# Kernel tuning notes

Hardware: AMD Instinct MI355X
Metric: run time of the kernel (lower is better)

Reference implementation:

```python
import jax, jax.numpy as jnp
import numpy as np

STRIDES = (8, 16, 32)
C = 80          # num_classes
KA = 3          # anchors per level
TOPK = 100      # per-level top-k
CONF_TH = 0.001
NMS_TH = 0.5
INPUT_SIZE = 2048
ANCHOR_SIZES = np.array([[[10, 13], [16, 30], [33, 23]],
                         [[30, 61], [62, 45], [59, 119]],
                         [[116, 90], [156, 198], [373, 326]]], dtype=np.float32)


def make_anchors(level):
    # Mirrors YOLOv3.create_grid: torch.meshgrid default is 'ij' indexing.
    fmp = INPUT_SIZE // STRIDES[level]
    gy, gx = np.meshgrid(np.arange(fmp), np.arange(fmp), indexing='ij')
    grid_xy = np.stack([gx, gy], axis=-1).reshape(-1, 1, 2).astype(np.float32)  # [HW,1,2]
    grid_xy = np.broadcast_to(grid_xy, (fmp * fmp, KA, 2))
    wh = np.broadcast_to(ANCHOR_SIZES[level][None], (fmp * fmp, KA, 2))
    return jnp.asarray(np.concatenate([grid_xy, wh], axis=-1).reshape(-1, 4))  # [HW*KA,4]


def setup_inputs() -> dict:
    key = jax.random.key(0)
    ks = jax.random.split(key, 9)
    d = {}
    for lvl in range(3):
        N = (INPUT_SIZE // STRIDES[lvl]) ** 2 * KA
        d[f"conf_pred_{lvl + 1}"] = jax.random.normal(ks[3 * lvl], (N, 1), jnp.float32)
        d[f"cls_pred_{lvl + 1}"] = jax.random.normal(ks[3 * lvl + 1], (N, C), jnp.float32)
        d[f"reg_pred_{lvl + 1}"] = jax.random.normal(ks[3 * lvl + 2], (N, 4), jnp.float32) * 0.5
        d[f"anchors_{lvl + 1}"] = make_anchors(lvl)
    return d


def _level(conf, cls, reg, anchors, stride):
    # scores = sigmoid(objectness) * softmax(class logits), flattened over (anchor, class)
    prob = jax.nn.sigmoid(conf) * jax.nn.softmax(cls, axis=-1)      # [N,C]
    scores, idx = jax.lax.top_k(prob.reshape(-1), TOPK)             # [TOPK]
    valid = scores > CONF_TH
    a_idx = idx // C
    labels = idx % C
    r = reg[a_idx]                                                  # [TOPK,4]
    a = anchors[a_idx]                                              # [TOPK,4]
    # decode_boxes: xy = (sigmoid(txy)+grid)*stride ; wh = exp(twh)*anchor_wh
    xy = (jax.nn.sigmoid(r[:, :2]) + a[:, :2]) * stride
    wh = jnp.exp(r[:, 2:]) * a[:, 2:]
    boxes = jnp.concatenate([xy - 0.5 * wh, xy + 0.5 * wh], axis=-1)  # x1y1x2y2
    return scores, labels, boxes, valid


def reference(conf_pred_1, cls_pred_1, reg_pred_1,
              conf_pred_2, cls_pred_2, reg_pred_2,
              conf_pred_3, cls_pred_3, reg_pred_3,
              anchors_1, anchors_2, anchors_3):
    levels = [(conf_pred_1, cls_pred_1, reg_pred_1, anchors_1, STRIDES[0]),
              (conf_pred_2, cls_pred_2, reg_pred_2, anchors_2, STRIDES[1]),
              (conf_pred_3, cls_pred_3, reg_pred_3, anchors_3, STRIDES[2])]
    parts = [_level(*lv) for lv in levels]
    scores = jnp.concatenate([p[0] for p in parts])   # [3*TOPK]
    labels = jnp.concatenate([p[1] for p in parts])
    boxes = jnp.concatenate([p[2] for p in parts], axis=0)
    valid = jnp.concatenate([p[3] for p in parts])

    # Sort all candidates by score descending (greedy NMS order)
    order = jnp.argsort(-scores)
    scores, labels, boxes, valid = scores[order], labels[order], boxes[order], valid[order]

    x1, y1, x2, y2 = boxes[:, 0], boxes[:, 1], boxes[:, 2], boxes[:, 3]
    areas = (x2 - x1) * (y2 - y1)
    xx1 = jnp.maximum(x1[:, None], x1[None, :])
    yy1 = jnp.maximum(y1[:, None], y1[None, :])
    xx2 = jnp.minimum(x2[:, None], x2[None, :])
    yy2 = jnp.minimum(y2[:, None], y2[None, :])
    w = jnp.maximum(1e-10, xx2 - xx1)
    h = jnp.maximum(1e-10, yy2 - yy1)
    inter = w * h
    iou = inter / (areas[:, None] + areas[None, :] - inter)

    K = scores.shape[0]
    idxr = jnp.arange(K)
    # class-wise suppression: only same-label, lower-scored boxes can be suppressed
    sup_cond = (iou > NMS_TH) & (labels[:, None] == labels[None, :]) & (idxr[None, :] > idxr[:, None])

    def body(i, keep):
        return keep & ~(sup_cond[i] & keep[i])

    keep = jax.lax.fori_loop(0, K, body, valid)

    boxes_n = jnp.clip(boxes / INPUT_SIZE, 0.0, 1.0)
    out = jnp.concatenate([boxes_n, scores[:, None], labels.astype(jnp.float32)[:, None]], axis=1)
    return jnp.where(keep[:, None], out, 0.0)   # [3*TOPK, 6] = (x1,y1,x2,y2,score,label)
```

## Files before the change

### kernel.cpp

```cpp
#include <hip/hip_runtime.h>
#include <math.h>
#include <stdint.h>

#define NBUCKET 4096
#define NCOPY   8
#define CAP     16384
#define QCAP    4096
#define STAGE   4096
#define FCAP    1024
#define TOPK    100
#define NLVL    3
#define NCLS    80

#define PA_G1 1024
#define PA_G2 256
#define PA_G3 64
#define CK_G1 192
#define CK_G2 48
#define CK_G3 12

__global__ void passA_kernel(const float* __restrict__ conf1, const float* __restrict__ cls1,
                             const float* __restrict__ conf2, const float* __restrict__ cls2,
                             const float* __restrict__ conf3, const float* __restrict__ cls3,
                             int n1, int n2, int n3,
                             unsigned int* __restrict__ ghist,
                             float* __restrict__ amax)
{
    const float* conf; const float* cls; int nA, nb, b;
    unsigned int* gh; float* am;
    if (blockIdx.x < PA_G1) {
        b = blockIdx.x; conf = conf1; cls = cls1; nA = n1; nb = PA_G1;
        gh = ghist; am = amax;
    } else if (blockIdx.x < PA_G1 + PA_G2) {
        b = blockIdx.x - PA_G1; conf = conf2; cls = cls2; nA = n2; nb = PA_G2;
        gh = ghist + NCOPY * NBUCKET; am = amax + n1;
    } else {
        b = blockIdx.x - PA_G1 - PA_G2; conf = conf3; cls = cls3; nA = n3; nb = PA_G3;
        gh = ghist + 2 * NCOPY * NBUCKET; am = amax + n1 + n2;
    }

    __shared__ unsigned int sh[NBUCKET];
    for (int i = threadIdx.x; i < NBUCKET; i += 256) sh[i] = 0;
    __syncthreads();

    int sub = threadIdx.x & 15;
    int g16 = threadIdx.x >> 4;
    int nChunk = nA >> 4;
    for (int ch = b; ch < nChunk; ch += nb) {
        int a = (ch << 4) + g16;
        float cv  = conf[a];
        float sig = 1.0f / (1.0f + expf(-cv));
        const float* row = cls + (size_t)a * NCLS + sub;
        float c0 = row[0], c1 = row[16], c2 = row[32], c3 = row[48], c4 = row[64];
        float m = fmaxf(fmaxf(fmaxf(c0, c1), fmaxf(c2, c3)), c4);
#pragma unroll
        for (int o = 8; o >= 1; o >>= 1) m = fmaxf(m, __shfl_xor(m, o, 16));
        float s = ((expf(c0 - m) + expf(c1 - m)) + (expf(c2 - m) + expf(c3 - m))) + expf(c4 - m);
#pragma unroll
        for (int o = 8; o >= 1; o >>= 1) s += __shfl_xor(s, o, 16);
        float inv = sig / s;
        if (sub == 0) {
            am[a] = inv;
            unsigned bk = __float_as_uint(inv) >> 18;
            if (bk > NBUCKET - 1) bk = NBUCKET - 1;
            atomicAdd(&sh[bk], 1u);
        }
    }
    __syncthreads();
    unsigned int* g = gh + (b & (NCOPY - 1)) * NBUCKET;
    for (int i = threadIdx.x; i < NBUCKET; i += 256) {
        unsigned v = sh[i];
        if (v) atomicAdd(&g[i], v);
    }
}

__global__ void scan_kernel(const unsigned int* __restrict__ ghist,
                            unsigned int* __restrict__ thresh,
                            unsigned int* __restrict__ ccount)
{
    int lvl = blockIdx.x;
    const unsigned int* h0 = ghist + lvl * NCOPY * NBUCKET;
    __shared__ unsigned int h[NBUCKET];
    __shared__ unsigned int ps[256];
    int t = threadIdx.x;
    if (t == 0) ccount[lvl] = 0;
    for (int bb = t; bb < NBUCKET; bb += 256) {
        unsigned s = 0;
        for (int c = 0; c < NCOPY; c++) s += h0[c * NBUCKET + bb];
        h[bb] = s;
    }
    __syncthreads();
    unsigned cs = 0;
#pragma unroll
    for (int i = 0; i < 16; i++) cs += h[NBUCKET - 1 - (t * 16 + i)];
    ps[t] = cs;
    __syncthreads();
    for (int o = 1; o < 256; o <<= 1) {
        unsigned v = (t >= o) ? ps[t - o] : 0u;
        __syncthreads();
        ps[t] += v;
        __syncthreads();
    }
    unsigned incl = ps[t], excl = incl - cs;
    if (excl < TOPK && incl >= TOPK) {
        unsigned cum = excl, B = 0;
        for (int i = 0; i < 16; i++) {
            int bb = NBUCKET - 1 - (t * 16 + i);
            cum += h[bb];
            if (cum >= TOPK) { B = (unsigned)bb; break; }
        }
        thresh[lvl] = B << 18;
    }
}

__global__ void compact_kernel(const float* __restrict__ conf1, const float* __restrict__ cls1,
                               const float* __restrict__ conf2, const float* __restrict__ cls2,
                               const float* __restrict__ conf3, const float* __restrict__ cls3,
                               int n1, int n2, int n3,
                               const unsigned int* __restrict__ thresh,
                               const float* __restrict__ amax,
                               unsigned int* __restrict__ ccount,
                               float* __restrict__ cscore,
                               unsigned int* __restrict__ cidx)
{
    const float* conf; const float* cls; int bl, lvl; const float* am;
    if (blockIdx.x < CK_G1)              { lvl = 0; bl = blockIdx.x;               conf = conf1; cls = cls1; am = amax; }
    else if (blockIdx.x < CK_G1 + CK_G2) { lvl = 1; bl = blockIdx.x - CK_G1;       conf = conf2; cls = cls2; am = amax + n1; }
    else                                 { lvl = 2; bl = blockIdx.x - CK_G1 - CK_G2; conf = conf3; cls = cls3; am = amax + n1 + n2; }

    __shared__ int qn;
    __shared__ int queue[QCAP];
    if (threadIdx.x == 0) qn = 0;
    __syncthreads();

    unsigned T = thresh[lvl];
    int idx4 = bl * 256 + threadIdx.x;
    const float4* am4 = (const float4*)am;
    float4 v = am4[idx4];
    float vv[4] = {v.x, v.y, v.z, v.w};
#pragma unroll
    for (int j = 0; j < 4; j++) {
        if (__float_as_uint(vv[j]) >= T) {
            int p = atomicAdd(&qn, 1);
            if (p < QCAP) queue[p] = idx4 * 4 + j;
        }
    }
    __syncthreads();
    int qcnt = min(qn, QCAP);
    int grp = threadIdx.x >> 4;
    int sub = threadIdx.x & 15;
    float*        csl = cscore + lvl * CAP;
    unsigned int* cil = cidx   + lvl * CAP;
    for (int q = grp; q < qcnt; q += 16) {
        int a = queue[q];
        float cv  = conf[a];
        float sig = 1.0f / (1.0f + expf(-cv));
        const float* row = cls + (size_t)a * NCLS + sub;
        float c0 = row[0], c1 = row[16], c2 = row[32], c3 = row[48], c4 = row[64];
        float m = fmaxf(fmaxf(fmaxf(c0, c1), fmaxf(c2, c3)), c4);
#pragma unroll
        for (int o = 8; o >= 1; o >>= 1) m = fmaxf(m, __shfl_xor(m, o, 16));
        float e0 = expf(c0 - m), e1 = expf(c1 - m), e2 = expf(c2 - m),
              e3 = expf(c3 - m), e4 = expf(c4 - m);
        float s = ((e0 + e1) + (e2 + e3)) + e4;
#pragma unroll
        for (int o = 8; o >= 1; o >>= 1) s += __shfl_xor(s, o, 16);
        float inv = sig / s;
        float e[5] = {e0, e1, e2, e3, e4};
#pragma unroll
        for (int k = 0; k < 5; k++) {
            float p = e[k] * inv;
            if (e[k] == 1.0f || __float_as_uint(p) >= T) {
                unsigned pos = atomicAdd(&ccount[lvl], 1u);
                if (pos < CAP) {
                    csl[pos] = p;
                    cil[pos] = (unsigned)(a * NCLS + sub + 16 * k);
                }
            }
        }
    }
}

__global__ __launch_bounds__(1024, 4) void select_kernel(
    const float* __restrict__ cscore, const unsigned int* __restrict__ cidx,
    const unsigned int* __restrict__ ccount,
    const unsigned int* __restrict__ thresh,
    float* __restrict__ sel_sc, int* __restrict__ sel_ix)
{
    int lvl = blockIdx.x;
    int tid = threadIdx.x;
    __shared__ float        q_sc[STAGE];
    __shared__ unsigned int q_ix[STAGE];
    __shared__ unsigned int subh[4096];
    __shared__ unsigned int ps[1024];
    __shared__ unsigned int kthr_s;
    __shared__ int          fcnt;
    __shared__ float        f_sc[FCAP];
    __shared__ unsigned int f_ix[FCAP];

    int cnt = min((int)ccount[lvl], CAP);
    const float*        sc = cscore + lvl * CAP;
    const unsigned int* ix = cidx   + lvl * CAP;
    int n = min(cnt, STAGE);
    unsigned B12 = (thresh[lvl] >> 18) << 12;

    for (int i = tid; i < 4096; i += 1024) subh[i] = 0;
    if (tid == 0) fcnt = 0;
    for (int c = tid; c < n; c += 1024) { q_sc[c] = sc[c]; q_ix[c] = ix[c]; }
    if (tid < TOPK) { sel_sc[lvl * TOPK + tid] = -1e30f; sel_ix[lvl * TOPK + tid] = 0; }
    __syncthreads();

    for (int c = tid; c < cnt; c += 1024) {
        float v = (c < n) ? q_sc[c] : sc[c];
        unsigned rel = (__float_as_uint(v) >> 6) - B12;
        if (rel > 4095u) rel = 4095u;
        atomicAdd(&subh[rel], 1u);
    }
    __syncthreads();

    unsigned cs = 0;
#pragma unroll
    for (int i = 0; i < 4; i++) cs += subh[4095 - 4 * tid - i];
    ps[tid] = cs;
    __syncthreads();
    for (int o = 1; o < 1024; o <<= 1) {
        unsigned v = (tid >= o) ? ps[tid - o] : 0u;
        __syncthreads();
        ps[tid] += v;
        __syncthreads();
    }
    {
        unsigned incl = ps[tid], excl = incl - cs;
        if (excl < TOPK && incl >= TOPK) {
            unsigned cum = excl;
            for (int i = 0; i < 4; i++) {
                int sb = 4095 - 4 * tid - i;
                cum += subh[sb];
                if (cum >= TOPK) { kthr_s = (B12 + (unsigned)sb) << 6; break; }
            }
        }
    }
    __syncthreads();
    unsigned kthr = kthr_s;

    for (int c = tid; c < cnt; c += 1024) {
        float v; unsigned vi;
        if (c < n) { v = q_sc[c]; vi = q_ix[c]; }
        else       { v = sc[c];   vi = ix[c];   }
        if (__float_as_uint(v) >= kthr) {
            int p = atomicAdd(&fcnt, 1);
            if (p < FCAP) { f_sc[p] = v; f_ix[p] = vi; }
        }
    }
    __syncthreads();
    int fn = min(fcnt, FCAP);

    for (int c = tid; c < fn; c += 1024) {
        float    my  = f_sc[c];
        unsigned myi = f_ix[c];
        int rank = 0;
        for (int k = 0; k < fn; k++) {
            float v = f_sc[k];
            rank += (v > my) || (v == my && f_ix[k] < myi);
        }
        if (rank < TOPK) {
            sel_sc[lvl * TOPK + rank] = my;
            sel_ix[lvl * TOPK + rank] = (int)myi;
        }
    }
}

__device__ __forceinline__ float rlf(float x, int l)
{
    return __uint_as_float((unsigned)__builtin_amdgcn_readlane((int)__float_as_uint(x), l));
}
__device__ __forceinline__ int rli(int x, int l)
{
    return __builtin_amdgcn_readlane(x, l);
}
__device__ __forceinline__ unsigned long long rl64(unsigned long long x, int b)
{
    unsigned lo = (unsigned)__builtin_amdgcn_readlane((int)(unsigned)x, b);
    unsigned hi = (unsigned)__builtin_amdgcn_readlane((int)(unsigned)(x >> 32), b);
    return ((unsigned long long)hi << 32) | lo;
}

__global__ void prep_kernel(
    const float* __restrict__ reg1, const float* __restrict__ anch1,
    const float* __restrict__ reg2, const float* __restrict__ anch2,
    const float* __restrict__ reg3, const float* __restrict__ anch3,
    const float* __restrict__ sel_sc, const int* __restrict__ sel_ix,
    float* __restrict__ t_score, float* __restrict__ t_box,
    int* __restrict__ t_label, int* __restrict__ t_valid)
{
    int tid  = threadIdx.x;
    int lane = tid & 63;

    float sg[5];
#pragma unroll
    for (int g = 0; g < 5; g++) {
        int k = g * 64 + lane;
        sg[g] = (k < 300) ? sel_sc[k] : -INFINITY;
    }

    float my = (tid < 300) ? sel_sc[tid] : -INFINITY;
    int rank = 0;
#pragma unroll
    for (int g = 0; g < 5; g++) {
        int base = g * 64;
#pragma unroll 1
        for (int ii = 0; ii < 64; ii++) {
            float v = rlf(sg[g], ii);
            int k = base + ii;
            rank += (v > my) || (v == my && k < tid);
        }
    }

    if (tid < 300) {
        int lvl = tid / TOPK;
        const float* reg = lvl == 0 ? reg1 : (lvl == 1 ? reg2 : reg3);
        const float* anc = lvl == 0 ? anch1 : (lvl == 1 ? anch2 : anch3);
        float stride = lvl == 0 ? 8.0f : (lvl == 1 ? 16.0f : 32.0f);
        int  idx = sel_ix[tid];
        int a   = idx / NCLS;
        int lab = idx % NCLS;
        float r0 = reg[4 * a + 0], r1 = reg[4 * a + 1], r2 = reg[4 * a + 2], r3 = reg[4 * a + 3];
        float a0 = anc[4 * a + 0], a1 = anc[4 * a + 1], a2 = anc[4 * a + 2], a3 = anc[4 * a + 3];
        float cx = (1.0f / (1.0f + expf(-r0)) + a0) * stride;
        float cy = (1.0f / (1.0f + expf(-r1)) + a1) * stride;
        float w  = expf(r2) * a2;
        float h  = expf(r3) * a3;
        t_score[rank]       = my;
        t_box[4 * rank + 0] = cx - 0.5f * w;
        t_box[4 * rank + 1] = cy - 0.5f * h;
        t_box[4 * rank + 2] = cx + 0.5f * w;
        t_box[4 * rank + 3] = cy + 0.5f * h;
        t_label[rank] = lab;
        t_valid[rank] = my > 0.001f;
    }
}

__global__ void sup_kernel(const float* __restrict__ t_box,
                           const int* __restrict__ t_label,
                           unsigned long long* __restrict__ sup_ws)
{
    int tid  = threadIdx.x;
    int lane = tid & 63;
    int w    = tid >> 6;
    int rbase = 20 * blockIdx.x;

    float bx1 = 0, by1 = 0, bx2 = 0, by2 = 0, areaj = 0;
    int labj = -1;
    if (tid < 300) {
        bx1 = t_box[4 * tid + 0]; by1 = t_box[4 * tid + 1];
        bx2 = t_box[4 * tid + 2]; by2 = t_box[4 * tid + 3];
        labj = t_label[tid];
        areaj = (bx2 - bx1) * (by2 - by1);
    }

    float rx1 = 0, ry1 = 0, rx2 = 0, ry2 = 0, rar = 1.0f;
    int rlab = -9;
    int r = rbase + lane;
    if (lane < 20 && r < 300) {
        rx1 = t_box[4 * r + 0]; ry1 = t_box[4 * r + 1];
        rx2 = t_box[4 * r + 2]; ry2 = t_box[4 * r + 3];
        rar = (rx2 - rx1) * (ry2 - ry1);
        rlab = t_label[r];
    }

#pragma unroll 1
    for (int ii = 0; ii < 20; ii++) {
        int i = rbase + ii;
        float xi1 = rlf(rx1, ii), yi1 = rlf(ry1, ii);
        float xi2 = rlf(rx2, ii), yi2 = rlf(ry2, ii);
        float ari = rlf(rar, ii);
        int  labi = rli(rlab, ii);
        float xx1 = fmaxf(xi1, bx1), yy1 = fmaxf(yi1, by1);
        float xx2 = fminf(xi2, bx2), yy2 = fminf(yi2, by2);
        float ww = fmaxf(1e-10f, xx2 - xx1);
        float hh = fmaxf(1e-10f, yy2 - yy1);
        float inter = ww * hh;
        float iou = inter / (ari + areaj - inter);
        bool p = (tid > i) && (labj == labi) && (iou > 0.5f) && (tid < 300);
        unsigned long long m = __ballot(p);
        if (lane == 0) sup_ws[i * 5 + w] = m;
    }
}

__global__ void nmsfin_kernel(const float* __restrict__ t_score,
                              const float* __restrict__ t_box,
                              const int* __restrict__ t_label,
                              const int* __restrict__ t_valid,
                              const unsigned long long* __restrict__ sup_ws,
                              float* __restrict__ out)
{
    int lane = threadIdx.x;

    unsigned long long s0[5], s1[5], s2[5], s3[5], s4[5];
#pragma unroll
    for (int q = 0; q < 5; q++) {
        s0[q] = sup_ws[(lane)       * 5 + q];
        s1[q] = sup_ws[(lane + 64)  * 5 + q];
        s2[q] = sup_ws[(lane + 128) * 5 + q];
        s3[q] = sup_ws[(lane + 192) * 5 + q];
        s4[q] = (lane + 256 < 300) ? sup_ws[(lane + 256) * 5 + q] : 0ull;
    }

    unsigned long long k0 = __ballot(t_valid[lane] != 0);
    unsigned long long k1 = __ballot(t_valid[lane + 64] != 0);
    unsigned long long k2 = __ballot(t_valid[lane + 128] != 0);
    unsigned long long k3 = __ballot(t_valid[lane + 192] != 0);
    unsigned long long k4 = __ballot((lane + 256 < 300) ? (t_valid[lane + 256] != 0) : false);

    unsigned long long nz0 = __ballot((s0[0] | s0[1] | s0[2] | s0[3] | s0[4]) != 0ull);
    unsigned long long nz1 = __ballot((s1[0] | s1[1] | s1[2] | s1[3] | s1[4]) != 0ull);
    unsigned long long nz2 = __ballot((s2[0] | s2[1] | s2[2] | s2[3] | s2[4]) != 0ull);
    unsigned long long nz3 = __ballot((s3[0] | s3[1] | s3[2] | s3[3] | s3[4]) != 0ull);
    unsigned long long nz4 = __ballot((s4[0] | s4[1] | s4[2] | s4[3] | s4[4]) != 0ull);

#define NMS_SPARSE(SR, KR, NZ)                                                \
    {                                                                         \
        unsigned long long m = (NZ);                                          \
        while (m) {                                                           \
            int b = __builtin_ctzll(m);                                       \
            m &= m - 1ull;                                                    \
            if ((KR >> b) & 1ull) {                                           \
                k0 &= ~rl64(SR[0], b);                                        \
                k1 &= ~rl64(SR[1], b);                                        \
                k2 &= ~rl64(SR[2], b);                                        \
                k3 &= ~rl64(SR[3], b);                                        \
                k4 &= ~rl64(SR[4], b);                                        \
            }                                                                 \
        }                                                                     \
    }
    NMS_SPARSE(s0, k0, nz0)
    NMS_SPARSE(s1, k1, nz1)
    NMS_SPARSE(s2, k2, nz2)
    NMS_SPARSE(s3, k3, nz3)
    NMS_SPARSE(s4, k4, nz4)
#undef NMS_SPARSE

#pragma unroll 1
    for (int e = lane; e < 300 * 6; e += 64) {
        int row = e / 6, col = e % 6;
        unsigned long long kw = (row < 64) ? k0 : (row < 128) ? k1 : (row < 192) ? k2
                              : (row < 256) ? k3 : k4;
        bool kept = (kw >> (row & 63)) & 1ull;
        float v = 0.0f;
        if (kept) {
            if (col < 4) {
                v = t_box[4 * row + col] * (1.0f / 2048.0f);
                v = fminf(fmaxf(v, 0.0f), 1.0f);
            } else if (col == 4) {
                v = t_score[row];
            } else {
                v = (float)t_label[row];
            }
        }
        out[e] = v;
    }
}

extern "C" void kernel_launch(void* const* d_in, const int* in_sizes, int n_in,
                              void* d_out, int out_size, void* d_ws, size_t ws_size,
                              hipStream_t stream)
{
    const float* conf1 = (const float*)d_in[0];
    const float* cls1  = (const float*)d_in[1];
    const float* reg1  = (const float*)d_in[2];
    const float* anch1 = (const float*)d_in[3];
    const float* conf2 = (const float*)d_in[4];
    const float* cls2  = (const float*)d_in[5];
    const float* reg2  = (const float*)d_in[6];
    const float* anch2 = (const float*)d_in[7];
    const float* conf3 = (const float*)d_in[8];
    const float* cls3  = (const float*)d_in[9];
    const float* reg3  = (const float*)d_in[10];
    const float* anch3 = (const float*)d_in[11];

    int N1 = in_sizes[0];
    int N2 = in_sizes[4];
    int N3 = in_sizes[8];

    unsigned int* wsu    = (unsigned int*)d_ws;
    unsigned int* hist   = wsu;
    unsigned int* thresh = wsu + NLVL * NCOPY * NBUCKET;
    unsigned int* ccount = thresh + NLVL;
    float*        amax   = (float*)(wsu + NLVL * NCOPY * NBUCKET + 16);
    float*        cscore = amax + (N1 + N2 + N3);
    unsigned int* cidx   = (unsigned int*)(cscore + NLVL * CAP);
    float*        sel_sc = (float*)(cidx + NLVL * CAP);
    int*          sel_ix = (int*)(sel_sc + NLVL * TOPK);
    float*        t_score = (float*)(sel_ix + NLVL * TOPK);
    float*        t_box   = t_score + 300;
    int*          t_label = (int*)(t_box + 1200);
    int*          t_valid = t_label + 300;
    unsigned long long* sup_ws =
        (unsigned long long*)(((uintptr_t)(t_valid + 300) + 15) & ~(uintptr_t)15);

    hipMemsetAsync(hist, 0, (size_t)(NLVL * NCOPY * NBUCKET) * sizeof(unsigned int), stream);

    passA_kernel<<<PA_G1 + PA_G2 + PA_G3, 256, 0, stream>>>(
        conf1, cls1, conf2, cls2, conf3, cls3, N1, N2, N3, hist, amax);

    scan_kernel<<<NLVL, 256, 0, stream>>>(hist, thresh, ccount);

    compact_kernel<<<CK_G1 + CK_G2 + CK_G3, 256, 0, stream>>>(
        conf1, cls1, conf2, cls2, conf3, cls3, N1, N2, N3,
        thresh, amax, ccount, cscore, cidx);

    select_kernel<<<NLVL, 1024, 0, stream>>>(cscore, cidx, ccount, thresh, sel_sc, sel_ix);

    prep_kernel<<<1, 320, 0, stream>>>(reg1, anch1, reg2, anch2, reg3, anch3,
                                       sel_sc, sel_ix, t_score, t_box, t_label, t_valid);

    sup_kernel<<<15, 320, 0, stream>>>(t_box, t_label, sup_ws);

    nmsfin_kernel<<<1, 64, 0, stream>>>(t_score, t_box, t_label, t_valid, sup_ws, (float*)d_out);
}
```

Measured before the change: 92.73 us.

## Fuse histogram scan, compaction and selection into one per-level block kernel

The global histogram, memset, scan kernel and multi-block compaction kernel are removed. A single 1024-thread block per level now builds the score histogram in LDS, finds the threshold, compacts candidate anchors and class scores into LDS, and runs the fine top-k selection. This drops three launches, the memset and the global atomics, and takes the histogram work out of the first pass. In exchange, all per-level scanning and class recomputation for the largest level runs on one workgroup, which reads the anchor maxima twice and may be bandwidth or latency bound on a single CU.

```diff
diff --git a/kernel.cpp b/kernel.cpp
--- a/kernel.cpp
+++ b/kernel.cpp
@@ -3,10 +3,8 @@
 #include <stdint.h>
 
 #define NBUCKET 4096
-#define NCOPY   8
-#define CAP     16384
-#define QCAP    4096
-#define STAGE   4096
+#define QCAP8   8192
+#define CAP2    8192
 #define FCAP    1024
 #define TOPK    100
 #define NLVL    3
@@ -15,33 +13,21 @@
 #define PA_G1 1024
 #define PA_G2 256
 #define PA_G3 64
-#define CK_G1 192
-#define CK_G2 48
-#define CK_G3 12
 
 __global__ void passA_kernel(const float* __restrict__ conf1, const float* __restrict__ cls1,
                              const float* __restrict__ conf2, const float* __restrict__ cls2,
                              const float* __restrict__ conf3, const float* __restrict__ cls3,
                              int n1, int n2, int n3,
-                             unsigned int* __restrict__ ghist,
                              float* __restrict__ amax)
 {
-    const float* conf; const float* cls; int nA, nb, b;
-    unsigned int* gh; float* am;
+    const float* conf; const float* cls; int nA, nb, b; float* am;
     if (blockIdx.x < PA_G1) {
-        b = blockIdx.x; conf = conf1; cls = cls1; nA = n1; nb = PA_G1;
-        gh = ghist; am = amax;
+        b = blockIdx.x; conf = conf1; cls = cls1; nA = n1; nb = PA_G1; am = amax;
     } else if (blockIdx.x < PA_G1 + PA_G2) {
-        b = blockIdx.x - PA_G1; conf = conf2; cls = cls2; nA = n2; nb = PA_G2;
-        gh = ghist + NCOPY * NBUCKET; am = amax + n1;
+        b = blockIdx.x - PA_G1; conf = conf2; cls = cls2; nA = n2; nb = PA_G2; am = amax + n1;
     } else {
-        b = blockIdx.x - PA_G1 - PA_G2; conf = conf3; cls = cls3; nA = n3; nb = PA_G3;
-        gh = ghist + 2 * NCOPY * NBUCKET; am = amax + n1 + n2;
-    }
-
-    __shared__ unsigned int sh[NBUCKET];
-    for (int i = threadIdx.x; i < NBUCKET; i += 256) sh[i] = 0;
-    __syncthreads();
+        b = blockIdx.x - PA_G1 - PA_G2; conf = conf3; cls = cls3; nA = n3; nb = PA_G3; am = amax + n1 + n2;
+    }
 
     int sub = threadIdx.x & 15;
     int g16 = threadIdx.x >> 4;
@@ -59,183 +45,159 @@
 #pragma unroll
         for (int o = 8; o >= 1; o >>= 1) s += __shfl_xor(s, o, 16);
         float inv = sig / s;
-        if (sub == 0) {
-            am[a] = inv;
-            unsigned bk = __float_as_uint(inv) >> 18;
-            if (bk > NBUCKET - 1) bk = NBUCKET - 1;
-            atomicAdd(&sh[bk], 1u);
-        }
-    }
-    __syncthreads();
-    unsigned int* g = gh + (b & (NCOPY - 1)) * NBUCKET;
-    for (int i = threadIdx.x; i < NBUCKET; i += 256) {
-        unsigned v = sh[i];
-        if (v) atomicAdd(&g[i], v);
-    }
-}
-
-__global__ void scan_kernel(const unsigned int* __restrict__ ghist,
-                            unsigned int* __restrict__ thresh,
-                            unsigned int* __restrict__ ccount)
-{
-    int lvl = blockIdx.x;
-    const unsigned int* h0 = ghist + lvl * NCOPY * NBUCKET;
-    __shared__ unsigned int h[NBUCKET];
-    __shared__ unsigned int ps[256];
-    int t = threadIdx.x;
-    if (t == 0) ccount[lvl] = 0;
-    for (int bb = t; bb < NBUCKET; bb += 256) {
-        unsigned s = 0;
-        for (int c = 0; c < NCOPY; c++) s += h0[c * NBUCKET + bb];
-        h[bb] = s;
-    }
-    __syncthreads();
-    unsigned cs = 0;
-#pragma unroll
-    for (int i = 0; i < 16; i++) cs += h[NBUCKET - 1 - (t * 16 + i)];
-    ps[t] = cs;
-    __syncthreads();
-    for (int o = 1; o < 256; o <<= 1) {
-        unsigned v = (t >= o) ? ps[t - o] : 0u;
-        __syncthreads();
-        ps[t] += v;
-        __syncthreads();
-    }
-    unsigned incl = ps[t], excl = incl - cs;
-    if (excl < TOPK && incl >= TOPK) {
-        unsigned cum = excl, B = 0;
-        for (int i = 0; i < 16; i++) {
-            int bb = NBUCKET - 1 - (t * 16 + i);
-            cum += h[bb];
-            if (cum >= TOPK) { B = (unsigned)bb; break; }
-        }
-        thresh[lvl] = B << 18;
-    }
-}
-
-__global__ void compact_kernel(const float* __restrict__ conf1, const float* __restrict__ cls1,
-                               const float* __restrict__ conf2, const float* __restrict__ cls2,
-                               const float* __restrict__ conf3, const float* __restrict__ cls3,
-                               int n1, int n2, int n3,
-                               const unsigned int* __restrict__ thresh,
-                               const float* __restrict__ amax,
-                               unsigned int* __restrict__ ccount,
-                               float* __restrict__ cscore,
-                               unsigned int* __restrict__ cidx)
-{
-    const float* conf; const float* cls; int bl, lvl; const float* am;
-    if (blockIdx.x < CK_G1)              { lvl = 0; bl = blockIdx.x;               conf = conf1; cls = cls1; am = amax; }
-    else if (blockIdx.x < CK_G1 + CK_G2) { lvl = 1; bl = blockIdx.x - CK_G1;       conf = conf2; cls = cls2; am = amax + n1; }
-    else                                 { lvl = 2; bl = blockIdx.x - CK_G1 - CK_G2; conf = conf3; cls = cls3; am = amax + n1 + n2; }
-
-    __shared__ int qn;
-    __shared__ int queue[QCAP];
-    if (threadIdx.x == 0) qn = 0;
-    __syncthreads();
-
-    unsigned T = thresh[lvl];
-    int idx4 = bl * 256 + threadIdx.x;
-    const float4* am4 = (const float4*)am;
-    float4 v = am4[idx4];
-    float vv[4] = {v.x, v.y, v.z, v.w};
-#pragma unroll
-    for (int j = 0; j < 4; j++) {
-        if (__float_as_uint(vv[j]) >= T) {
-            int p = atomicAdd(&qn, 1);
-            if (p < QCAP) queue[p] = idx4 * 4 + j;
-        }
-    }
-    __syncthreads();
-    int qcnt = min(qn, QCAP);
-    int grp = threadIdx.x >> 4;
-    int sub = threadIdx.x & 15;
-    float*        csl = cscore + lvl * CAP;
-    unsigned int* cil = cidx   + lvl * CAP;
-    for (int q = grp; q < qcnt; q += 16) {
-        int a = queue[q];
-        float cv  = conf[a];
-        float sig = 1.0f / (1.0f + expf(-cv));
-        const float* row = cls + (size_t)a * NCLS + sub;
-        float c0 = row[0], c1 = row[16], c2 = row[32], c3 = row[48], c4 = row[64];
-        float m = fmaxf(fmaxf(fmaxf(c0, c1), fmaxf(c2, c3)), c4);
-#pragma unroll
-        for (int o = 8; o >= 1; o >>= 1) m = fmaxf(m, __shfl_xor(m, o, 16));
-        float e0 = expf(c0 - m), e1 = expf(c1 - m), e2 = expf(c2 - m),
-              e3 = expf(c3 - m), e4 = expf(c4 - m);
-        float s = ((e0 + e1) + (e2 + e3)) + e4;
-#pragma unroll
-        for (int o = 8; o >= 1; o >>= 1) s += __shfl_xor(s, o, 16);
-        float inv = sig / s;
-        float e[5] = {e0, e1, e2, e3, e4};
-#pragma unroll
-        for (int k = 0; k < 5; k++) {
-            float p = e[k] * inv;
-            if (e[k] == 1.0f || __float_as_uint(p) >= T) {
-                unsigned pos = atomicAdd(&ccount[lvl], 1u);
-                if (pos < CAP) {
-                    csl[pos] = p;
-                    cil[pos] = (unsigned)(a * NCLS + sub + 16 * k);
-                }
-            }
-        }
-    }
-}
-
-__global__ __launch_bounds__(1024, 4) void select_kernel(
-    const float* __restrict__ cscore, const unsigned int* __restrict__ cidx,
-    const unsigned int* __restrict__ ccount,
-    const unsigned int* __restrict__ thresh,
+        if (sub == 0) am[a] = inv;
+    }
+}
+
+__global__ __launch_bounds__(1024, 1) void fsel_kernel(
+    const float* __restrict__ conf1, const float* __restrict__ cls1,
+    const float* __restrict__ conf2, const float* __restrict__ cls2,
+    const float* __restrict__ conf3, const float* __restrict__ cls3,
+    int n1, int n2, int n3,
+    const float* __restrict__ amax,
     float* __restrict__ sel_sc, int* __restrict__ sel_ix)
 {
     int lvl = blockIdx.x;
     int tid = threadIdx.x;
-    __shared__ float        q_sc[STAGE];
-    __shared__ unsigned int q_ix[STAGE];
-    __shared__ unsigned int subh[4096];
+
+    const float* conf; const float* cls; const float* am; int nA;
+    if (lvl == 0)      { conf = conf1; cls = cls1; am = amax;            nA = n1; }
+    else if (lvl == 1) { conf = conf2; cls = cls2; am = amax + n1;       nA = n2; }
+    else               { conf = conf3; cls = cls3; am = amax + n1 + n2;  nA = n3; }
+
+    __shared__ unsigned int hist[NBUCKET];
     __shared__ unsigned int ps[1024];
+    __shared__ unsigned int thr_s;
+    __shared__ int          qn;
+    __shared__ int          queue[QCAP8];
+    __shared__ int          ccnt;
+    __shared__ float        c_sc[CAP2];
+    __shared__ unsigned int c_ix[CAP2];
     __shared__ unsigned int kthr_s;
     __shared__ int          fcnt;
     __shared__ float        f_sc[FCAP];
     __shared__ unsigned int f_ix[FCAP];
 
-    int cnt = min((int)ccount[lvl], CAP);
-    const float*        sc = cscore + lvl * CAP;
-    const unsigned int* ix = cidx   + lvl * CAP;
-    int n = min(cnt, STAGE);
-    unsigned B12 = (thresh[lvl] >> 18) << 12;
-
-    for (int i = tid; i < 4096; i += 1024) subh[i] = 0;
-    if (tid == 0) fcnt = 0;
-    for (int c = tid; c < n; c += 1024) { q_sc[c] = sc[c]; q_ix[c] = ix[c]; }
+    for (int i = tid; i < NBUCKET; i += 1024) hist[i] = 0;
+    if (tid == 0) { qn = 0; ccnt = 0; fcnt = 0; }
     if (tid < TOPK) { sel_sc[lvl * TOPK + tid] = -1e30f; sel_ix[lvl * TOPK + tid] = 0; }
     __syncthreads();
 
-    for (int c = tid; c < cnt; c += 1024) {
-        float v = (c < n) ? q_sc[c] : sc[c];
-        unsigned rel = (__float_as_uint(v) >> 6) - B12;
-        if (rel > 4095u) rel = 4095u;
-        atomicAdd(&subh[rel], 1u);
-    }
-    __syncthreads();
-
-    unsigned cs = 0;
-#pragma unroll
-    for (int i = 0; i < 4; i++) cs += subh[4095 - 4 * tid - i];
-    ps[tid] = cs;
-    __syncthreads();
-    for (int o = 1; o < 1024; o <<= 1) {
-        unsigned v = (tid >= o) ? ps[tid - o] : 0u;
+    const float4* am4 = (const float4*)am;
+    int n4 = nA >> 2;
+    for (int i = tid; i < n4; i += 1024) {
+        float4 v = am4[i];
+        float vv[4] = {v.x, v.y, v.z, v.w};
+#pragma unroll
+        for (int j = 0; j < 4; j++) {
+            unsigned bk = __float_as_uint(vv[j]) >> 18;
+            if (bk > NBUCKET - 1) bk = NBUCKET - 1;
+            atomicAdd(&hist[bk], 1u);
+        }
+    }
+    __syncthreads();
+
+    {
+        unsigned cs = 0;
+#pragma unroll
+        for (int i = 0; i < 4; i++) cs += hist[NBUCKET - 1 - 4 * tid - i];
+        ps[tid] = cs;
         __syncthreads();
-        ps[tid] += v;
-        __syncthreads();
-    }
-    {
+        for (int o = 1; o < 1024; o <<= 1) {
+            unsigned v = (tid >= o) ? ps[tid - o] : 0u;
+            __syncthreads();
+            ps[tid] += v;
+            __syncthreads();
+        }
         unsigned incl = ps[tid], excl = incl - cs;
         if (excl < TOPK && incl >= TOPK) {
             unsigned cum = excl;
             for (int i = 0; i < 4; i++) {
-                int sb = 4095 - 4 * tid - i;
-                cum += subh[sb];
+                int bb = NBUCKET - 1 - 4 * tid - i;
+                cum += hist[bb];
+                if (cum >= TOPK) { thr_s = (unsigned)bb << 18; break; }
+            }
+        }
+    }
+    __syncthreads();
+    unsigned T = thr_s;
+    unsigned B12 = (T >> 18) << 12;
+
+    for (int i = tid; i < n4; i += 1024) {
+        float4 v = am4[i];
+        float vv[4] = {v.x, v.y, v.z, v.w};
+#pragma unroll
+        for (int j = 0; j < 4; j++) {
+            if (__float_as_uint(vv[j]) >= T) {
+                int p = atomicAdd(&qn, 1);
+                if (p < QCAP8) queue[p] = i * 4 + j;
+            }
+        }
+    }
+    __syncthreads();
+    int qcnt = min(qn, QCAP8);
+
+    {
+        int grp = tid >> 4;
+        int sub = tid & 15;
+        for (int q = grp; q < qcnt; q += 64) {
+            int a = queue[q];
+            float cv  = conf[a];
+            float sig = 1.0f / (1.0f + expf(-cv));
+            const float* row = cls + (size_t)a * NCLS + sub;
+            float c0 = row[0], c1 = row[16], c2 = row[32], c3 = row[48], c4 = row[64];
+            float m = fmaxf(fmaxf(fmaxf(c0, c1), fmaxf(c2, c3)), c4);
+#pragma unroll
+            for (int o = 8; o >= 1; o >>= 1) m = fmaxf(m, __shfl_xor(m, o, 16));
+            float e0 = expf(c0 - m), e1 = expf(c1 - m), e2 = expf(c2 - m),
+                  e3 = expf(c3 - m), e4 = expf(c4 - m);
+            float s = ((e0 + e1) + (e2 + e3)) + e4;
+#pragma unroll
+            for (int o = 8; o >= 1; o >>= 1) s += __shfl_xor(s, o, 16);
+            float inv = sig / s;
+            float e[5] = {e0, e1, e2, e3, e4};
+#pragma unroll
+            for (int k = 0; k < 5; k++) {
+                float p = e[k] * inv;
+                if (e[k] == 1.0f || __float_as_uint(p) >= T) {
+                    int pos = atomicAdd(&ccnt, 1);
+                    if (pos < CAP2) {
+                        c_sc[pos] = p;
+                        c_ix[pos] = (unsigned)(a * NCLS + sub + 16 * k);
+                    }
+                }
+            }
+        }
+    }
+    __syncthreads();
+    int cnt = min(ccnt, CAP2);
+
+    for (int i = tid; i < NBUCKET; i += 1024) hist[i] = 0;
+    __syncthreads();
+    for (int c = tid; c < cnt; c += 1024) {
+        unsigned rel = (__float_as_uint(c_sc[c]) >> 6) - B12;
+        if (rel > 4095u) rel = 4095u;
+        atomicAdd(&hist[rel], 1u);
+    }
+    __syncthreads();
+    {
+        unsigned cs = 0;
+#pragma unroll
+        for (int i = 0; i < 4; i++) cs += hist[NBUCKET - 1 - 4 * tid - i];
+        ps[tid] = cs;
+        __syncthreads();
+        for (int o = 1; o < 1024; o <<= 1) {
+            unsigned v = (tid >= o) ? ps[tid - o] : 0u;
+            __syncthreads();
+            ps[tid] += v;
+            __syncthreads();
+        }
+        unsigned incl = ps[tid], excl = incl - cs;
+        if (excl < TOPK && incl >= TOPK) {
+            unsigned cum = excl;
+            for (int i = 0; i < 4; i++) {
+                int sb = NBUCKET - 1 - 4 * tid - i;
+                cum += hist[sb];
                 if (cum >= TOPK) { kthr_s = (B12 + (unsigned)sb) << 6; break; }
             }
         }
@@ -244,12 +206,10 @@
     unsigned kthr = kthr_s;
 
     for (int c = tid; c < cnt; c += 1024) {
-        float v; unsigned vi;
-        if (c < n) { v = q_sc[c]; vi = q_ix[c]; }
-        else       { v = sc[c];   vi = ix[c];   }
+        float v = c_sc[c];
         if (__float_as_uint(v) >= kthr) {
             int p = atomicAdd(&fcnt, 1);
-            if (p < FCAP) { f_sc[p] = v; f_ix[p] = vi; }
+            if (p < FCAP) { f_sc[p] = v; f_ix[p] = c_ix[c]; }
         }
     }
     __syncthreads();
@@ -482,14 +442,8 @@
     int N2 = in_sizes[4];
     int N3 = in_sizes[8];
 
-    unsigned int* wsu    = (unsigned int*)d_ws;
-    unsigned int* hist   = wsu;
-    unsigned int* thresh = wsu + NLVL * NCOPY * NBUCKET;
-    unsigned int* ccount = thresh + NLVL;
-    float*        amax   = (float*)(wsu + NLVL * NCOPY * NBUCKET + 16);
-    float*        cscore = amax + (N1 + N2 + N3);
-    unsigned int* cidx   = (unsigned int*)(cscore + NLVL * CAP);
-    float*        sel_sc = (float*)(cidx + NLVL * CAP);
+    float*        amax   = (float*)d_ws;
+    float*        sel_sc = amax + (N1 + N2 + N3);
     int*          sel_ix = (int*)(sel_sc + NLVL * TOPK);
     float*        t_score = (float*)(sel_ix + NLVL * TOPK);
     float*        t_box   = t_score + 300;
@@ -498,18 +452,11 @@
     unsigned long long* sup_ws =
         (unsigned long long*)(((uintptr_t)(t_valid + 300) + 15) & ~(uintptr_t)15);
 
-    hipMemsetAsync(hist, 0, (size_t)(NLVL * NCOPY * NBUCKET) * sizeof(unsigned int), stream);
-
     passA_kernel<<<PA_G1 + PA_G2 + PA_G3, 256, 0, stream>>>(
-        conf1, cls1, conf2, cls2, conf3, cls3, N1, N2, N3, hist, amax);
-
-    scan_kernel<<<NLVL, 256, 0, stream>>>(hist, thresh, ccount);
-
-    compact_kernel<<<CK_G1 + CK_G2 + CK_G3, 256, 0, stream>>>(
-        conf1, cls1, conf2, cls2, conf3, cls3, N1, N2, N3,
-        thresh, amax, ccount, cscore, cidx);
-
-    select_kernel<<<NLVL, 1024, 0, stream>>>(cscore, cidx, ccount, thresh, sel_sc, sel_ix);
+        conf1, cls1, conf2, cls2, conf3, cls3, N1, N2, N3, amax);
+
+    fsel_kernel<<<NLVL, 1024, 0, stream>>>(
+        conf1, cls1, conf2, cls2, conf3, cls3, N1, N2, N3, amax, sel_sc, sel_ix);
 
     prep_kernel<<<1, 320, 0, stream>>>(reg1, anch1, reg2, anch2, reg3, anch3,
                                        sel_sc, sel_ix, t_score, t_box, t_label, t_valid);
```

Measured after the change: 101.5 us. +9.5%, slower.
